# Optimization experiments

Measured on AMD Instinct MI355X. Metric: run time of the kernel, lower is better.

The kernel has to match this reference:

```python
import jax, jax.numpy as jnp
import numpy as np

B, D = 512, 1024
NK, DIMS = 160, 3  # hardcoded in the layer: Dense(160*3), reshape (-1,160,3)


def setup_inputs() -> dict:
    key = jax.random.key(0)
    k1, k2 = jax.random.split(key)
    inputs = jax.random.normal(k1, (B, D), dtype=jnp.float32)
    W = jax.random.normal(k2, (D, NK * DIMS), dtype=jnp.float32) * 0.02
    b = jnp.zeros((NK * DIMS,), dtype=jnp.float32)
    return {"inputs": inputs, "W": W, "b": b}


def reference(inputs, W, b):
    # dense projection: [B, D] @ [D, 480] -> [B, 480]
    x = inputs @ W + b
    act = x.reshape(-1, NK, DIMS)                       # [B, 160, 3]
    # pairwise diffs: [B, 160, 3, 1] - [1, 160, 3, B] -> [B, 160, 3, B]
    diffs = act[:, :, :, None] - jnp.transpose(act, (1, 2, 0))[None]
    abs_diffs = jnp.sum(jnp.abs(diffs), axis=2)         # [B, 160, B]
    minibatch_features = jnp.sum(jnp.exp(-abs_diffs), axis=2)  # [B, 160]
    return jnp.concatenate([inputs, minibatch_features], axis=1)  # [B, D+160]
```

## Files before the change

### kernel.cpp

```cpp
#include <hip/hip_runtime.h>
#include <hip/hip_bf16.h>

#define B_SZ 512
#define D_SZ 1024
#define NK 160
#define NCOL 480
#define OUTW 1184
#define LOG2E 1.44269504088896340736f
#define PLANE 245760

typedef __attribute__((ext_vector_type(8))) short bf16x8;
typedef __attribute__((ext_vector_type(4))) float f32x4;

__device__ __forceinline__ unsigned int f32_bf16_rne(float f) {
    unsigned int u = __float_as_uint(f);
    u += 0x7fffu + ((u >> 16) & 1u);
    return u >> 16;
}
__device__ __forceinline__ unsigned int pk2(float x, float y) {
    return f32_bf16_rne(x) | (f32_bf16_rne(y) << 16);
}

__global__ __launch_bounds__(256, 2) void mbd_gemm_kernel(
    const float* __restrict__ A,
    const float* __restrict__ W,
    const float* __restrict__ bias,
    float* __restrict__ act2)
{
    __shared__ char lds[65536];
    const int bid = blockIdx.x;
    const int xcd = bid & 7, loc = bid >> 3;
    const int bm = xcd * 2 + (loc & 1);
    const int ksp = (loc >> 1) & 1;
    const int bn = loc >> 2;
    const int i0 = bm * 32, c0 = bn * 32, kb0 = ksp * 512;
    const int t = threadIdx.x;
    const int w = __builtin_amdgcn_readfirstlane(t >> 6);
    const int l = t & 63, lhi = l >> 4, llo = l & 15;

    const int arow = t >> 3, aseg = t & 7;
    const int aswz = (arow & 7) << 4;
    const float* __restrict__ aptr = A + (size_t)(i0 + arow) * D_SZ + kb0 + aseg * 4;
    const int kp8 = t >> 3, cq = t & 7;
    const float* __restrict__ wbase = W + (size_t)(kb0 + 2 * kp8) * NCOL + c0 + 4 * cq;

    float4 ra[16], rw0[8], rw1[8];
#pragma unroll
    for (int q = 0; q < 16; ++q)
        ra[q] = *reinterpret_cast<const float4*>(aptr + q * 32);
#pragma unroll
    for (int m = 0; m < 8; ++m) {
        rw0[m] = *reinterpret_cast<const float4*>(wbase + (size_t)(64 * m) * NCOL);
        rw1[m] = *reinterpret_cast<const float4*>(wbase + (size_t)(64 * m + 1) * NCOL);
    }

    {
        char* arp = lds + arow * 1024;
#pragma unroll
        for (int q = 0; q < 16; ++q) {
            uint2 p;
            p.x = pk2(ra[q].x, ra[q].y);
            p.y = pk2(ra[q].z, ra[q].w);
            *reinterpret_cast<uint2*>(arp + ((aseg * 8 + 64 * q) ^ aswz)) = p;
        }
#pragma unroll
        for (int m = 0; m < 8; ++m) {
            const int p = kp8 + 32 * m;
#pragma unroll
            for (int j = 0; j < 4; ++j) {
                const int col = 4 * cq + j;
                const float v0 = (&rw0[m].x)[j];
                const float v1 = (&rw1[m].x)[j];
                *reinterpret_cast<unsigned int*>(
                    lds + 32768 + col * 1024 + ((4 * p) ^ ((col & 7) << 4))) = pk2(v0, v1);
            }
        }
    }
    __syncthreads();

    f32x4 acc = {0.f, 0.f, 0.f, 0.f};
    const int r0 = (w & 1) * 16, cc = (w >> 1) * 16;
    const int lswz = (llo & 7) << 4;
#pragma unroll
    for (int m = 0; m < 16; ++m) {
        const int koff = (lhi * 16 + m * 64) ^ lswz;
        const bf16x8 af = *reinterpret_cast<const bf16x8*>(lds + (r0 + llo) * 1024 + koff);
        const bf16x8 bf = *reinterpret_cast<const bf16x8*>(lds + 32768 + (cc + llo) * 1024 + koff);
        acc = __builtin_amdgcn_mfma_f32_16x16x32_bf16(af, bf, acc, 0, 0, 0);
    }

    const int col = c0 + cc + llo;
    const float bs = ksp ? 0.f : bias[col];
    float4 o;
    o.x = (acc[0] + bs) * LOG2E;
    o.y = (acc[1] + bs) * LOG2E;
    o.z = (acc[2] + bs) * LOG2E;
    o.w = (acc[3] + bs) * LOG2E;
    *reinterpret_cast<float4*>(
        &act2[(size_t)ksp * PLANE + (size_t)col * B_SZ + i0 + r0 + lhi * 4]) = o;
}

__global__ __launch_bounds__(256) void mbd_pairwise_kernel(
    const float* __restrict__ act2,
    float* __restrict__ feat_t)
{
    __shared__ float4 as4[B_SZ];
    const int bid = blockIdx.x;
    const int t = threadIdx.x;

    const int klin = (bid & 7) * 80 + (bid >> 3);
    const int k = klin >> 2;
    const int c = klin & 3;

    const float* __restrict__ p0 = act2 + (size_t)(3 * k + 0) * B_SZ;
    const float* __restrict__ p1 = act2 + (size_t)(3 * k + 1) * B_SZ;
    const float* __restrict__ p2 = act2 + (size_t)(3 * k + 2) * B_SZ;
#pragma unroll
    for (int s = 0; s < 2; ++s) {
        const int idx = t + s * 256;
        as4[idx] = make_float4(p0[idx] + p0[idx + PLANE],
                               p1[idx] + p1[idx + PLANE],
                               p2[idx] + p2[idx + PLANE], 0.f);
    }
    __syncthreads();

    const int w = t >> 6, lane = t & 63;
    const int rg = lane & 3;
    const int jq = lane >> 2;
    const int r0 = c * 128 + w * 32 + rg * 8;

    float ax[8], ay[8], az[8], acc[8];
#pragma unroll
    for (int i = 0; i < 8; ++i) {
        const float4 v = as4[r0 + i];
        ax[i] = v.x; ay[i] = v.y; az[i] = v.z;
        acc[i] = 0.f;
    }

#pragma unroll 4
    for (int jj = 0; jj < 32; ++jj) {
        const float4 av = as4[jq + jj * 16];
#pragma unroll
        for (int i = 0; i < 8; ++i)
            acc[i] += __builtin_amdgcn_exp2f(
                -(fabsf(ax[i] - av.x) + fabsf(ay[i] - av.y) + fabsf(az[i] - av.z)));
    }
#pragma unroll
    for (int m = 4; m <= 32; m <<= 1) {
#pragma unroll
        for (int i = 0; i < 8; ++i) acc[i] += __shfl_xor(acc[i], m);
    }
    if (lane < 4) {
#pragma unroll
        for (int i = 0; i < 8; ++i)
            feat_t[(size_t)k * B_SZ + r0 + i] = acc[i];
    }
}

__global__ __launch_bounds__(64) void mbd_copyout_kernel(
    const float* __restrict__ A,
    const float* __restrict__ feat_t,
    float* __restrict__ out)
{
    const int i = blockIdx.x;
    const int t = threadIdx.x;
#pragma unroll
    for (int s = 0; s < 4; ++s) {
        const int c4 = (t + s * 64) * 4;
        const float4 v = *reinterpret_cast<const float4*>(&A[i * D_SZ + c4]);
        *reinterpret_cast<float4*>(&out[i * OUTW + c4]) = v;
    }
    out[i * OUTW + D_SZ + t]      = feat_t[(size_t)t * B_SZ + i];
    out[i * OUTW + D_SZ + t + 64] = feat_t[(size_t)(t + 64) * B_SZ + i];
    if (t < 32)
        out[i * OUTW + D_SZ + t + 128] = feat_t[(size_t)(t + 128) * B_SZ + i];
}

extern "C" void kernel_launch(void* const* d_in, const int* in_sizes, int n_in,
                              void* d_out, int out_size, void* d_ws, size_t ws_size,
                              hipStream_t stream)
{
    const float* inputs = (const float*)d_in[0];
    const float* W      = (const float*)d_in[1];
    const float* bias   = (const float*)d_in[2];
    float* out = (float*)d_out;

    char* ws = (char*)d_ws;
    float* act2   = (float*)ws;
    float* feat_t = (float*)(ws + 1966080);

    mbd_gemm_kernel<<<480, 256, 0, stream>>>(inputs, W, bias, act2);
    mbd_pairwise_kernel<<<640, 256, 0, stream>>>(act2, feat_t);
    mbd_copyout_kernel<<<B_SZ, 64, 0, stream>>>(inputs, feat_t, out);
}
```

Before: 25.56 us.

## Exploit pairwise symmetry with upper-triangular tiles and atomic row/column accumulation

The pairwise kernel now computes only the upper-triangular 64x64 tile pairs per kernel (36 of 64) and adds each exp term to both the row and the column sums, using the symmetry of the L1 distance to roughly halve the exp work. Results are accumulated with atomicAdd into a row-major feat buffer, which the GEMM kernel zeroes beforehand. The output kernel then reads feat contiguously instead of transposing. The cost is many small 64-thread blocks, atomic traffic, and a serial loop to decode tile indices.

```diff
diff --git a/kernel.cpp b/kernel.cpp
--- a/kernel.cpp
+++ b/kernel.cpp
@@ -25,16 +25,20 @@
     const float* __restrict__ A,
     const float* __restrict__ W,
     const float* __restrict__ bias,
-    float* __restrict__ act2)
+    float* __restrict__ act2,
+    float* __restrict__ feat)
 {
     __shared__ char lds[65536];
     const int bid = blockIdx.x;
+    const int t = threadIdx.x;
+
+    if (bid < 320) feat[bid * 256 + t] = 0.f;
+
     const int xcd = bid & 7, loc = bid >> 3;
     const int bm = xcd * 2 + (loc & 1);
     const int ksp = (loc >> 1) & 1;
     const int bn = loc >> 2;
     const int i0 = bm * 32, c0 = bn * 32, kb0 = ksp * 512;
-    const int t = threadIdx.x;
     const int w = __builtin_amdgcn_readfirstlane(t >> 6);
     const int l = t & 63, lhi = l >> 4, llo = l & 15;
 
@@ -100,66 +104,80 @@
         &act2[(size_t)ksp * PLANE + (size_t)col * B_SZ + i0 + r0 + lhi * 4]) = o;
 }
 
-__global__ __launch_bounds__(256) void mbd_pairwise_kernel(
+__global__ __launch_bounds__(64) void mbd_pairsym_kernel(
     const float* __restrict__ act2,
-    float* __restrict__ feat_t)
-{
-    __shared__ float4 as4[B_SZ];
+    float* __restrict__ feat)
+{
+    __shared__ float4 as4[128];
     const int bid = blockIdx.x;
+    const int lin = (bid & 7) * 720 + (bid >> 3);
+    const int k = lin / 36;
+    int p = lin % 36;
+    int ci = 0;
+    while (p >= 8 - ci) { p -= 8 - ci; ++ci; }
+    const int cj = ci + p;
     const int t = threadIdx.x;
-
-    const int klin = (bid & 7) * 80 + (bid >> 3);
-    const int k = klin >> 2;
-    const int c = klin & 3;
 
     const float* __restrict__ p0 = act2 + (size_t)(3 * k + 0) * B_SZ;
     const float* __restrict__ p1 = act2 + (size_t)(3 * k + 1) * B_SZ;
     const float* __restrict__ p2 = act2 + (size_t)(3 * k + 2) * B_SZ;
-#pragma unroll
-    for (int s = 0; s < 2; ++s) {
-        const int idx = t + s * 256;
-        as4[idx] = make_float4(p0[idx] + p0[idx + PLANE],
-                               p1[idx] + p1[idx + PLANE],
-                               p2[idx] + p2[idx + PLANE], 0.f);
+    {
+        const int ra = ci * 64 + t;
+        as4[t] = make_float4(p0[ra] + p0[ra + PLANE],
+                             p1[ra] + p1[ra + PLANE],
+                             p2[ra] + p2[ra + PLANE], 0.f);
+        const int rb = cj * 64 + t;
+        as4[64 + t] = make_float4(p0[rb] + p0[rb + PLANE],
+                                  p1[rb] + p1[rb + PLANE],
+                                  p2[rb] + p2[rb + PLANE], 0.f);
     }
     __syncthreads();
 
-    const int w = t >> 6, lane = t & 63;
-    const int rg = lane & 3;
-    const int jq = lane >> 2;
-    const int r0 = c * 128 + w * 32 + rg * 8;
-
-    float ax[8], ay[8], az[8], acc[8];
+    const int a = t & 7;
+    const int b = t >> 3;
+    float rx[8], ry[8], rz[8], ar[8], ac[8];
 #pragma unroll
     for (int i = 0; i < 8; ++i) {
-        const float4 v = as4[r0 + i];
-        ax[i] = v.x; ay[i] = v.y; az[i] = v.z;
-        acc[i] = 0.f;
-    }
-
-#pragma unroll 4
-    for (int jj = 0; jj < 32; ++jj) {
-        const float4 av = as4[jq + jj * 16];
-#pragma unroll
-        for (int i = 0; i < 8; ++i)
-            acc[i] += __builtin_amdgcn_exp2f(
-                -(fabsf(ax[i] - av.x) + fabsf(ay[i] - av.y) + fabsf(az[i] - av.z)));
-    }
-#pragma unroll
-    for (int m = 4; m <= 32; m <<= 1) {
-#pragma unroll
-        for (int i = 0; i < 8; ++i) acc[i] += __shfl_xor(acc[i], m);
-    }
-    if (lane < 4) {
-#pragma unroll
-        for (int i = 0; i < 8; ++i)
-            feat_t[(size_t)k * B_SZ + r0 + i] = acc[i];
-    }
-}
-
-__global__ __launch_bounds__(64) void mbd_copyout_kernel(
+        const float4 v = as4[a * 8 + i];
+        rx[i] = v.x; ry[i] = v.y; rz[i] = v.z;
+        ar[i] = 0.f; ac[i] = 0.f;
+    }
+
+#pragma unroll
+    for (int c = 0; c < 8; ++c) {
+        const float4 cv = as4[64 + b * 8 + c];
+#pragma unroll
+        for (int r = 0; r < 8; ++r) {
+            const float e = __builtin_amdgcn_exp2f(
+                -(fabsf(rx[r] - cv.x) + fabsf(ry[r] - cv.y) + fabsf(rz[r] - cv.z)));
+            ar[r] += e;
+            ac[c] += e;
+        }
+    }
+#pragma unroll
+    for (int m = 8; m <= 32; m <<= 1)
+#pragma unroll
+        for (int i = 0; i < 8; ++i) ar[i] += __shfl_xor(ar[i], m);
+#pragma unroll
+    for (int m = 1; m <= 4; m <<= 1)
+#pragma unroll
+        for (int i = 0; i < 8; ++i) ac[i] += __shfl_xor(ac[i], m);
+
+    if (b == 0) {
+#pragma unroll
+        for (int r = 0; r < 8; ++r)
+            atomicAdd(&feat[(size_t)(ci * 64 + a * 8 + r) * NK + k], ar[r]);
+    }
+    if (ci != cj && a == 0) {
+#pragma unroll
+        for (int c = 0; c < 8; ++c)
+            atomicAdd(&feat[(size_t)(cj * 64 + b * 8 + c) * NK + k], ac[c]);
+    }
+}
+
+__global__ __launch_bounds__(64) void mbd_out_kernel(
     const float* __restrict__ A,
-    const float* __restrict__ feat_t,
+    const float* __restrict__ feat,
     float* __restrict__ out)
 {
     const int i = blockIdx.x;
@@ -170,10 +188,12 @@
         const float4 v = *reinterpret_cast<const float4*>(&A[i * D_SZ + c4]);
         *reinterpret_cast<float4*>(&out[i * OUTW + c4]) = v;
     }
-    out[i * OUTW + D_SZ + t]      = feat_t[(size_t)t * B_SZ + i];
-    out[i * OUTW + D_SZ + t + 64] = feat_t[(size_t)(t + 64) * B_SZ + i];
-    if (t < 32)
-        out[i * OUTW + D_SZ + t + 128] = feat_t[(size_t)(t + 128) * B_SZ + i];
+#pragma unroll
+    for (int s = 0; s < 3; ++s) {
+        const int idx = t + s * 64;
+        if (idx < NK)
+            out[i * OUTW + D_SZ + idx] = feat[(size_t)i * NK + idx];
+    }
 }
 
 extern "C" void kernel_launch(void* const* d_in, const int* in_sizes, int n_in,
@@ -186,10 +206,10 @@
     float* out = (float*)d_out;
 
     char* ws = (char*)d_ws;
-    float* act2   = (float*)ws;
-    float* feat_t = (float*)(ws + 1966080);
-
-    mbd_gemm_kernel<<<480, 256, 0, stream>>>(inputs, W, bias, act2);
-    mbd_pairwise_kernel<<<640, 256, 0, stream>>>(act2, feat_t);
-    mbd_copyout_kernel<<<B_SZ, 64, 0, stream>>>(inputs, feat_t, out);
-}
+    float* act2 = (float*)ws;
+    float* feat = (float*)(ws + 1966080);
+
+    mbd_gemm_kernel<<<480, 256, 0, stream>>>(inputs, W, bias, act2, feat);
+    mbd_pairsym_kernel<<<160 * 36, 64, 0, stream>>>(act2, feat);
+    mbd_out_kernel<<<B_SZ, 64, 0, stream>>>(inputs, feat, out);
+}
```

New measurement: 50.07 us. 95.9% more time.
